# Performance work log

Hardware: AMD Instinct MI355X
Metric: run time of the kernel (lower is better)

The kernel has to match this reference:

```python
import jax, jax.numpy as jnp
import numpy as np

D_K = 64  # key/query head dim used for the 1/sqrt(d_k) scale


def setup_inputs() -> dict:
    key0 = jax.random.key(0)
    kk, kq, kv = jax.random.split(key0, 3)
    B, H, S, DK, DV = 2, 16, 2048, 64, 64
    return {
        "key": jax.random.normal(kk, (B, H, S, DK), dtype=jnp.float32),
        "query": jax.random.normal(kq, (B, H, S, DK), dtype=jnp.float32),
        "value": jax.random.normal(kv, (B, H, S, DV), dtype=jnp.float32),
    }


def reference(key, query, value):
    # scaled dot-product attention per head: [B,H,S,S]
    scores = jnp.einsum("bhqd,bhkd->bhqk", query, key) / jnp.sqrt(jnp.asarray(D_K, query.dtype))
    attn = jax.nn.softmax(scores, axis=-1)
    out = jnp.einsum("bhqk,bhkv->bhqv", attn, value)  # [B,H,S,d_v]
    B, H, S, DV = out.shape
    # faithful to the torch .view: raw reshape (no head transpose)
    return out.reshape(B, S, H * DV)
```

## Files before the change

### kernel.cpp

```cpp
#include <hip/hip_runtime.h>

#define S_LEN 2048
#define DHEAD 64
#define BHEADS 32
#define NTILES 32
#define HEAD_ELEMS (S_LEN * DHEAD)
#define TENS_ELEMS (BHEADS * HEAD_ELEMS)
#define TILE_HALVES 4096

typedef _Float16 half8_t __attribute__((ext_vector_type(8)));
typedef _Float16 half4_t __attribute__((ext_vector_type(4)));
typedef _Float16 half2_t __attribute__((ext_vector_type(2)));
typedef float float4_t __attribute__((ext_vector_type(4)));

#define SC_LOG2E 0.18033688011112042f


__global__ __launch_bounds__(256) void prep_kernel(const float* __restrict__ K,
                                                   const float* __restrict__ V,
                                                   _Float16* __restrict__ Kf,
                                                   _Float16* __restrict__ Vf) {
    __shared__ _Float16 tile[64][72];
    const int bh = blockIdx.x >> 5;
    const int t = blockIdx.x & 31;
    const int tid = threadIdx.x;

    const float* Ksrc = K + (bh * S_LEN + t * 64) * DHEAD;
    const float4* vs = (const float4*)(V + (bh * S_LEN + t * 64) * DHEAD);
#pragma unroll
    for (int it = 0; it < 4; ++it) {
        int i = it * 256 + tid;
        float4 vv = vs[i];
        int r = i >> 4, c4 = (i & 15) * 4;
        half4_t hv = {(_Float16)vv.x, (_Float16)vv.y, (_Float16)vv.z, (_Float16)vv.w};
        *(half4_t*)&tile[r][c4] = hv;
    }

    _Float16* kd = Kf + (bh * NTILES + t) * TILE_HALVES;
#pragma unroll
    for (int it = 0; it < 2; ++it) {
        int c = it * 256 + tid;
        int f = c >> 6, lane = c & 63;
        int row = (f >> 1) * 16 + (lane & 15);
        int d0 = (f & 1) * 32 + (lane >> 4) * 8;
        const float4* s = (const float4*)(Ksrc + row * DHEAD + d0);
        float4 a = s[0], b = s[1];
        half8_t h = {(_Float16)(a.x * SC_LOG2E), (_Float16)(a.y * SC_LOG2E),
                     (_Float16)(a.z * SC_LOG2E), (_Float16)(a.w * SC_LOG2E),
                     (_Float16)(b.x * SC_LOG2E), (_Float16)(b.y * SC_LOG2E),
                     (_Float16)(b.z * SC_LOG2E), (_Float16)(b.w * SC_LOG2E)};
        *(half8_t*)(kd + c * 8) = h;
    }
    __syncthreads();

    _Float16* vd = Vf + (bh * NTILES + t) * TILE_HALVES;
#pragma unroll
    for (int it = 0; it < 2; ++it) {
        int c = it * 256 + tid;
        int fv = c >> 6, lane = c & 63;
        int vt = fv >> 1, ktp = fv & 1;
        int v = vt * 16 + (lane & 15);
        int g = lane >> 4;
        half8_t h;
#pragma unroll
        for (int j = 0; j < 8; ++j) {
            int key = ktp * 32 + (j >> 2) * 16 + g * 4 + (j & 3);
            h[j] = tile[key][v];
        }
        *(half8_t*)(vd + c * 8) = h;
    }
}


__global__ __launch_bounds__(256, 2) void attn_kernel(
    const float* __restrict__ Qf,
    const _Float16* __restrict__ Kf,
    const _Float16* __restrict__ Vf,
    float* __restrict__ out) {
    __shared__ float red[2][68][64];

    const int tid = threadIdx.x;
    const int wid = tid >> 6;
    const int lane = tid & 63;
    const int ln15 = lane & 15;
    const int g = lane >> 4;

    const int bh = blockIdx.x & 31;
    const int qidx = blockIdx.x >> 5;
    const int qg = wid >> 1;
    const int ks = wid & 1;
    const int q0 = qidx * 128 + qg * 64;
    const int t0 = ks * 16;

    const float* Qg = Qf + (bh * S_LEN + q0) * DHEAD;
    half8_t qf[4][2];
#pragma unroll
    for (int nq = 0; nq < 4; ++nq)
#pragma unroll
        for (int kh = 0; kh < 2; ++kh) {
            const float4* qs = (const float4*)(Qg + (nq * 16 + ln15) * DHEAD + kh * 32 + g * 8);
            float4 a = qs[0], b = qs[1];
            qf[nq][kh] = (half8_t){(_Float16)a.x, (_Float16)a.y, (_Float16)a.z, (_Float16)a.w,
                                   (_Float16)b.x, (_Float16)b.y, (_Float16)b.z, (_Float16)b.w};
        }

    const _Float16* kb = Kf + bh * (NTILES * TILE_HALVES) + t0 * TILE_HALVES;
    const _Float16* vb = Vf + bh * (NTILES * TILE_HALVES) + t0 * TILE_HALVES;
    const int lo = lane * 8;

    float lsum[4] = {0.f, 0.f, 0.f, 0.f};
    float4_t o[4][4];
#pragma unroll
    for (int nq = 0; nq < 4; ++nq)
#pragma unroll
        for (int vt = 0; vt < 4; ++vt) o[nq][vt] = (float4_t){0.f, 0.f, 0.f, 0.f};

#pragma unroll 2
    for (int t = 0; t < 16; ++t) {
        const int base = t * TILE_HALVES;
        half8_t kf[8], vf[8];
#pragma unroll
        for (int f = 0; f < 8; ++f) kf[f] = *(const half8_t*)(kb + base + f * 512 + lo);
#pragma unroll
        for (int f = 0; f < 8; ++f) vf[f] = *(const half8_t*)(vb + base + f * 512 + lo);

#pragma unroll
        for (int c = 0; c < 2; ++c) {
            half8_t pb[4];
#pragma unroll
            for (int h = 0; h < 2; ++h) {
                const int mt = 2 * c + h;
                half8_t a0 = kf[mt * 2];
                half8_t a1 = kf[mt * 2 + 1];
#pragma unroll
                for (int nq = 0; nq < 4; ++nq) {
                    float4_t c0 = (float4_t){0.f, 0.f, 0.f, 0.f};
                    c0 = __builtin_amdgcn_mfma_f32_16x16x32_f16(a0, qf[nq][0], c0, 0, 0, 0);
                    c0 = __builtin_amdgcn_mfma_f32_16x16x32_f16(a1, qf[nq][1], c0, 0, 0, 0);
                    float p0 = __builtin_amdgcn_exp2f(c0[0]);
                    float p1 = __builtin_amdgcn_exp2f(c0[1]);
                    float p2 = __builtin_amdgcn_exp2f(c0[2]);
                    float p3 = __builtin_amdgcn_exp2f(c0[3]);
                    lsum[nq] += (p0 + p1) + (p2 + p3);
                    half2_t plo = __builtin_bit_cast(half2_t, __builtin_amdgcn_cvt_pkrtz(p0, p1));
                    half2_t phi = __builtin_bit_cast(half2_t, __builtin_amdgcn_cvt_pkrtz(p2, p3));
                    pb[nq][h * 4 + 0] = plo[0];
                    pb[nq][h * 4 + 1] = plo[1];
                    pb[nq][h * 4 + 2] = phi[0];
                    pb[nq][h * 4 + 3] = phi[1];
                }
            }
#pragma unroll
            for (int vt = 0; vt < 4; ++vt) {
                half8_t va = vf[vt * 2 + c];
#pragma unroll
                for (int nq = 0; nq < 4; ++nq)
                    o[nq][vt] = __builtin_amdgcn_mfma_f32_16x16x32_f16(va, pb[nq], o[nq][vt], 0, 0, 0);
            }
        }
    }

#pragma unroll
    for (int nq = 0; nq < 4; ++nq) {
        float l = lsum[nq];
        l += __shfl_xor(l, 16, 64);
        l += __shfl_xor(l, 32, 64);
        lsum[nq] = l;
    }

    if (ks == 1) {
#pragma unroll
        for (int nq = 0; nq < 4; ++nq)
#pragma unroll
            for (int vt = 0; vt < 4; ++vt)
#pragma unroll
                for (int r = 0; r < 4; ++r)
                    red[qg][nq * 16 + vt * 4 + r][lane] = o[nq][vt][r];
#pragma unroll
        for (int nq = 0; nq < 4; ++nq) red[qg][64 + nq][lane] = lsum[nq];
    }
    __syncthreads();
    if (ks == 0) {
#pragma unroll
        for (int nq = 0; nq < 4; ++nq) {
            float lt = lsum[nq] + red[qg][64 + nq][lane];
            float inv_l = 1.0f / lt;
            int qg_global = q0 + nq * 16 + ln15;
            float* og = out + (bh * S_LEN + qg_global) * DHEAD;
#pragma unroll
            for (int vt = 0; vt < 4; ++vt) {
                float4_t vals;
#pragma unroll
                for (int r = 0; r < 4; ++r)
                    vals[r] = (o[nq][vt][r] + red[qg][nq * 16 + vt * 4 + r][lane]) * inv_l;
                *(float4_t*)(og + vt * 16 + g * 4) = vals;
            }
        }
    }
}


extern "C" void kernel_launch(void* const* d_in, const int* in_sizes, int n_in,
                              void* d_out, int out_size, void* d_ws, size_t ws_size,
                              hipStream_t stream) {
    const float* Kin = (const float*)d_in[0];
    const float* Qin = (const float*)d_in[1];
    const float* Vin = (const float*)d_in[2];
    float* out = (float*)d_out;

    _Float16* Kf = (_Float16*)d_ws;
    _Float16* Vf = Kf + TENS_ELEMS;

    prep_kernel<<<BHEADS * NTILES, 256, 0, stream>>>(Kin, Vin, Kf, Vf);
    attn_kernel<<<BHEADS * 16, 256, 0, stream>>>(Qin, Kf, Vf, out);
}
```

Measured before the change: 127.0 us.

## Double-buffer K/V tiles in LDS via direct global-to-LDS loads

K and V tiles are now staged into shared memory with global_load_lds, double-buffered. Waves sharing the same key split cooperatively load the K and V halves, so each wave reads both from LDS instead of each wave loading them from global memory. The intent is to halve redundant global traffic and overlap the next tile's load with compute. The cost is a block-wide barrier every iteration, and 64KB of LDS per block, which may limit occupancy to 2 blocks per CU. The reduction buffer is aliased onto the same LDS.

```diff
diff --git a/kernel.cpp b/kernel.cpp
--- a/kernel.cpp
+++ b/kernel.cpp
@@ -15,6 +15,12 @@
 
 #define SC_LOG2E 0.18033688011112042f
 
+
+typedef const __attribute__((address_space(1))) unsigned int gas_u32;
+typedef __attribute__((address_space(3))) unsigned int las_u32;
+__device__ __forceinline__ void stage16(const void* g, void* l) {
+    __builtin_amdgcn_global_load_lds((gas_u32*)g, (las_u32*)l, 16, 0, 0);
+}
 
 __global__ __launch_bounds__(256) void prep_kernel(const float* __restrict__ K,
                                                    const float* __restrict__ V,
@@ -77,7 +83,9 @@
     const _Float16* __restrict__ Kf,
     const _Float16* __restrict__ Vf,
     float* __restrict__ out) {
-    __shared__ float red[2][68][64];
+    __shared__ __align__(16) char smem[65536];
+    _Float16 (*kv)[2][2][TILE_HALVES] = (_Float16 (*)[2][2][TILE_HALVES])smem;
+    float (*red)[68][64] = (float (*)[68][64])smem;
 
     const int tid = threadIdx.x;
     const int wid = tid >> 6;
@@ -108,6 +116,8 @@
     const _Float16* vb = Vf + bh * (NTILES * TILE_HALVES) + t0 * TILE_HALVES;
     const int lo = lane * 8;
 
+    const _Float16* gstage = (qg == 0) ? kb : vb;
+
     float lsum[4] = {0.f, 0.f, 0.f, 0.f};
     float4_t o[4][4];
 #pragma unroll
@@ -115,14 +125,33 @@
 #pragma unroll
         for (int vt = 0; vt < 4; ++vt) o[nq][vt] = (float4_t){0.f, 0.f, 0.f, 0.f};
 
+    {
+        _Float16* ld = &kv[ks][0][qg][0];
+#pragma unroll
+        for (int f = 0; f < 8; ++f)
+            stage16(gstage + f * 512 + lo, ld + f * 512);
+    }
+    __syncthreads();
+
 #pragma unroll 2
     for (int t = 0; t < 16; ++t) {
-        const int base = t * TILE_HALVES;
+        const int buf = t & 1;
+
+        if (t < 15) {
+            const _Float16* gs = gstage + (t + 1) * TILE_HALVES + lo;
+            _Float16* ld = &kv[ks][buf ^ 1][qg][0];
+#pragma unroll
+            for (int f = 0; f < 8; ++f)
+                stage16(gs + f * 512, ld + f * 512);
+        }
+
+        const _Float16* kl = &kv[ks][buf][0][0];
+        const _Float16* vl = &kv[ks][buf][1][0];
         half8_t kf[8], vf[8];
 #pragma unroll
-        for (int f = 0; f < 8; ++f) kf[f] = *(const half8_t*)(kb + base + f * 512 + lo);
-#pragma unroll
-        for (int f = 0; f < 8; ++f) vf[f] = *(const half8_t*)(vb + base + f * 512 + lo);
+        for (int f = 0; f < 8; ++f) kf[f] = *(const half8_t*)(kl + f * 512 + lo);
+#pragma unroll
+        for (int f = 0; f < 8; ++f) vf[f] = *(const half8_t*)(vl + f * 512 + lo);
 
 #pragma unroll
         for (int c = 0; c < 2; ++c) {
@@ -158,6 +187,8 @@
                     o[nq][vt] = __builtin_amdgcn_mfma_f32_16x16x32_f16(va, pb[nq], o[nq][vt], 0, 0, 0);
             }
         }
+
+        __syncthreads();
     }
 
 #pragma unroll
```

After: 128.3 us. Within noise of the previous version (+1.0%).
